# Kernel optimization log

Hardware: AMD Instinct MI355X
Metric: run time of the kernel (lower is better)

Reference implementation:

```python
import jax, jax.numpy as jnp
import numpy as np

N, E = 40000, 640000
EMB, HID, H, TXT = 128, 128, 4, 384
C = HID // H  # per-head channels = 32


def _prelu(x, a):
    return jnp.where(x >= 0, x, a * x)


def _layernorm(x, g, b, eps=1e-5):
    m = jnp.mean(x, axis=-1, keepdims=True)
    v = jnp.mean((x - m) ** 2, axis=-1, keepdims=True)
    return (x - m) / jnp.sqrt(v + eps) * g + b


def _gat_conv(h, src, dst, W, att_src, att_dst, bias):
    # PyG GATConv (concat=True, eval mode): lin has no bias, self-loops already in src/dst.
    xh = (h @ W.T).reshape(N, H, C)                      # [N,H,C]
    a_src = jnp.sum(xh * att_src, axis=-1)               # [N,H]
    a_dst = jnp.sum(xh * att_dst, axis=-1)               # [N,H]
    alpha = jax.nn.leaky_relu(a_src[src] + a_dst[dst], negative_slope=0.2)  # [Et,H]
    amax = jax.ops.segment_max(alpha, dst, num_segments=N)
    ex = jnp.exp(alpha - amax[dst])
    denom = jax.ops.segment_sum(ex, dst, num_segments=N)
    coef = ex / denom[dst]                               # scatter-softmax over dst
    out = jax.ops.segment_sum(xh[src] * coef[:, :, None], dst, num_segments=N)
    return out.reshape(N, H * C) + bias


def setup_inputs() -> dict:
    key = jax.random.key(0)
    ks = jax.random.split(key, 20)
    nrm = lambda k, s, sc=0.05: jax.random.normal(k, s, jnp.float32) * sc
    inp = {
        "x": nrm(ks[0], (N, EMB), 1.0),
        "num_x": nrm(ks[1], (N, 1), 1.0),
        "num_mask": jnp.ones((N,), jnp.float32),
        "txt_x": nrm(ks[2], (N, TXT), 1.0),
        "txt_mask": jnp.ones((N,), jnp.float32),
        "edge_index": jax.random.randint(ks[3], (2, E), 0, N, jnp.int32),
        "num_proj_w": nrm(ks[4], (EMB, 1)), "num_proj_b": jnp.zeros((EMB,), jnp.float32),
        "txt_proj_w": nrm(ks[5], (EMB, TXT)), "txt_proj_b": jnp.zeros((EMB,), jnp.float32),
        "node_proj_w": nrm(ks[6], (HID, EMB)), "node_proj_b": jnp.zeros((HID,), jnp.float32),
        "prelu0_a": jnp.full((HID,), 0.25, jnp.float32),
        "conv1_w": nrm(ks[7], (HID, HID)), "att_src1": nrm(ks[8], (H, C)), "att_dst1": nrm(ks[9], (H, C)), "bias1": jnp.zeros((HID,), jnp.float32),
        "norm1_g": jnp.ones((HID,), jnp.float32), "norm1_b": jnp.zeros((HID,), jnp.float32),
        "prelu1_a": jnp.full((HID,), 0.25, jnp.float32),
        "conv2_w": nrm(ks[10], (HID, HID)), "att_src2": nrm(ks[11], (H, C)), "att_dst2": nrm(ks[12], (H, C)), "bias2": jnp.zeros((HID,), jnp.float32),
        "norm2_g": jnp.ones((HID,), jnp.float32), "norm2_b": jnp.zeros((HID,), jnp.float32),
        "prelu2_a": jnp.full((HID,), 0.25, jnp.float32),
        "out_w": nrm(ks[13], (1, HID)), "out_b": jnp.zeros((1,), jnp.float32),
    }
    return inp


def reference(x, num_x, num_mask, txt_x, txt_mask, edge_index,
              num_proj_w, num_proj_b, txt_proj_w, txt_proj_b,
              node_proj_w, node_proj_b, prelu0_a,
              conv1_w, att_src1, att_dst1, bias1, norm1_g, norm1_b, prelu1_a,
              conv2_w, att_src2, att_dst2, bias2, norm2_g, norm2_b, prelu2_a,
              out_w, out_b):
    # add self loops (PyG GATConv default)
    loop = jnp.arange(N, dtype=edge_index.dtype)
    src = jnp.concatenate([edge_index[0], loop])
    dst = jnp.concatenate([edge_index[1], loop])

    h = (num_x * num_mask[:, None]) @ num_proj_w.T + num_proj_b
    h = h + (txt_x * txt_mask[:, None]) @ txt_proj_w.T + txt_proj_b
    h = h + x @ node_proj_w.T + node_proj_b
    h = _prelu(h, prelu0_a)

    h = _gat_conv(h, src, dst, conv1_w, att_src1, att_dst1, bias1)
    h = _prelu(_layernorm(h, norm1_g, norm1_b), prelu1_a)  # dropout: eval mode -> identity

    h = _gat_conv(h, src, dst, conv2_w, att_src2, att_dst2, bias2)
    h = _prelu(_layernorm(h, norm2_g, norm2_b), prelu2_a)

    return (h @ out_w.T + out_b).squeeze(-1)  # [N]
```

## Files before the change

kernel.cpp:

```cpp
#include <hip/hip_runtime.h>
#include <stdint.h>

typedef unsigned short u16;
typedef unsigned int u32;
typedef __attribute__((ext_vector_type(8))) short bf16x8;
typedef __attribute__((ext_vector_type(4))) float f32x4;

__device__ __forceinline__ float bf2f(u32 u) {
    union { u32 i; float f; } v; v.i = u << 16; return v.f;
}
__device__ __forceinline__ u16 f2bf(float f) {
    u32 x = __float_as_uint(f);
    return (u16)((x + 0x7fffu + ((x >> 16) & 1u)) >> 16);
}
__device__ __forceinline__ float wred_sum(float v) {
#pragma unroll
    for (int o = 32; o > 0; o >>= 1) v += __shfl_xor(v, o, 64);
    return v;
}
__device__ __forceinline__ bf16x8 ldA_f32(const float* p, size_t off) {
    union { uint4 u; bf16x8 b; } t;
    const float* af = p + off;
    float4 a = *(const float4*)af, b2 = *(const float4*)(af + 4);
    t.u.x = (u32)f2bf(a.x)  | ((u32)f2bf(a.y)  << 16);
    t.u.y = (u32)f2bf(a.z)  | ((u32)f2bf(a.w)  << 16);
    t.u.z = (u32)f2bf(b2.x) | ((u32)f2bf(b2.y) << 16);
    t.u.w = (u32)f2bf(b2.z) | ((u32)f2bf(b2.w) << 16);
    return t.b;
}
__device__ __forceinline__ bf16x8 ld16B(const u16* p, size_t off) {
    union { uint4 u; bf16x8 b; } t; t.u = *(const uint4*)(p + off); return t.b;
}
__device__ __forceinline__ bf16x8 ldB(const u16* sw, int ct, int ks, int l16, int quad) {
    union { uint4 u; bf16x8 b; } t;
    t.u = *(const uint4*)&sw[(ct * 16 + l16) * 136 + ks * 32 + quad * 8];
    return t.b;
}
__device__ __forceinline__ void stage256_f32(const float* W, int stride, int koff,
                                             u16* sw, int tid) {
#pragma unroll
    for (int it = 0; it < 8; ++it) {
        int idx = (it * 256 + tid) * 8;
        int c = idx >> 7, kk = idx & 127;
        const float* wf = W + (size_t)c * stride + koff + kk;
        float4 a = *(const float4*)wf, b = *(const float4*)(wf + 4);
        uint4 v;
        v.x = (u32)f2bf(a.x) | ((u32)f2bf(a.y) << 16);
        v.y = (u32)f2bf(a.z) | ((u32)f2bf(a.w) << 16);
        v.z = (u32)f2bf(b.x) | ((u32)f2bf(b.y) << 16);
        v.w = (u32)f2bf(b.z) | ((u32)f2bf(b.w) << 16);
        *(uint4*)&sw[c * 136 + kk] = v;
    }
}

__global__ void k_zero(int* __restrict__ p, int n) {
    int i = blockIdx.x * 256 + threadIdx.x;
    if (i < n) p[i] = 0;
}
__global__ void k_hist(const int* __restrict__ dst, int E, int* __restrict__ deg) {
    int e = blockIdx.x * 256 + threadIdx.x;
    if (e < E) atomicAdd(&deg[dst[e]], 1);
}
__global__ __launch_bounds__(1024) void k_scanA(const int* __restrict__ deg, int n,
                                                int* __restrict__ out, int* __restrict__ bsum) {
    __shared__ int wsum[16];
    int t = threadIdx.x, w = t >> 6, lane = t & 63;
    int i0 = blockIdx.x * 4096 + t * 4;
    int4 v = make_int4(0, 0, 0, 0);
    if (i0 + 3 < n) v = *(const int4*)&deg[i0];
    else {
        if (i0 < n)     v.x = deg[i0];
        if (i0 + 1 < n) v.y = deg[i0 + 1];
        if (i0 + 2 < n) v.z = deg[i0 + 2];
    }
    int tsum = v.x + v.y + v.z + v.w;
    int s = tsum;
#pragma unroll
    for (int o = 1; o < 64; o <<= 1) { int u = __shfl_up(s, o, 64); if (lane >= o) s += u; }
    if (lane == 63) wsum[w] = s;
    __syncthreads();
    if (w == 0 && lane < 16) {
        int ws = wsum[lane];
#pragma unroll
        for (int o = 1; o < 16; o <<= 1) { int u = __shfl_up(ws, o, 64); if (lane >= o) ws += u; }
        wsum[lane] = ws;
    }
    __syncthreads();
    int woff = (w == 0) ? 0 : wsum[w - 1];
    int p = woff + s - tsum;
    if (i0 + 3 < n) {
        int4 o4; o4.x = p; o4.y = p + v.x; o4.z = p + v.x + v.y; o4.w = p + v.x + v.y + v.z;
        *(int4*)&out[i0] = o4;
    } else {
        int pp = p;
        if (i0 < n)     { out[i0] = pp;     pp += v.x; }
        if (i0 + 1 < n) { out[i0 + 1] = pp; pp += v.y; }
        if (i0 + 2 < n) { out[i0 + 2] = pp; }
    }
    if (t == 0) bsum[blockIdx.x] = wsum[15];
}
__global__ void k_scanB(int* __restrict__ bsum, int nb, int* __restrict__ total) {
    int lane = threadIdx.x;
    int v = (lane < nb) ? bsum[lane] : 0;
    int s = v;
#pragma unroll
    for (int o = 1; o < 64; o <<= 1) { int u = __shfl_up(s, o, 64); if (lane >= o) s += u; }
    if (lane < nb) bsum[lane] = s - v;
    if (lane == 63) total[0] = s;
}
__global__ void k_scanC(int* __restrict__ rowptr, int* __restrict__ cursor,
                        const int* __restrict__ boff, int n) {
    int i = blockIdx.x * 256 + threadIdx.x;
    if (i < n) {
        int r = rowptr[i] + boff[i >> 12];
        rowptr[i] = r; cursor[i] = r;
    }
}
__global__ void k_scatter(const int* __restrict__ srcp, const int* __restrict__ dstp, int E,
                          int* __restrict__ cursor, int* __restrict__ col) {
    int e = blockIdx.x * 256 + threadIdx.x;
    if (e < E) {
        int p = atomicAdd(&cursor[dstp[e]], 1);
        col[p] = srcp[e];
    }
}

__global__ __launch_bounds__(256) void k_fused1(
    const float* __restrict__ x, const float* __restrict__ numx, const float* __restrict__ numm,
    const float* __restrict__ txt, const float* __restrict__ txtm,
    const float* __restrict__ numw, const float* __restrict__ numb,
    const float* __restrict__ txtw, const float* __restrict__ txtb,
    const float* __restrict__ nodew, const float* __restrict__ nodeb,
    const float* __restrict__ pa,
    const float* __restrict__ W1, const float* __restrict__ atts, const float* __restrict__ attd,
    u16* __restrict__ xh, float* __restrict__ asrc, float* __restrict__ adst) {
    __shared__ u16 sw[128 * 136];
    __shared__ u16 sh[4][16 * 136];
    int tid = threadIdx.x, w = tid >> 6, lane = tid & 63, quad = lane >> 4, l16 = lane & 15;
    int nb = blockIdx.x * 64 + w * 16;
    f32x4 acc[8];
#pragma unroll
    for (int ct = 0; ct < 8; ++ct) { f32x4 z = {0.f, 0.f, 0.f, 0.f}; acc[ct] = z; }

    for (int chunk = 0; chunk < 3; ++chunk) {
        __syncthreads();
        stage256_f32(txtw, 384, chunk * 128, sw, tid);
        __syncthreads();
#pragma unroll
        for (int ks = 0; ks < 4; ++ks) {
            bf16x8 a0 = ldA_f32(txt, (size_t)(nb + l16) * 384 + chunk * 128 + ks * 32 + quad * 8);
#pragma unroll
            for (int ct = 0; ct < 8; ++ct)
                acc[ct] = __builtin_amdgcn_mfma_f32_16x16x32_bf16(
                    a0, ldB(sw, ct, ks, l16, quad), acc[ct], 0, 0, 0);
        }
    }
#pragma unroll
    for (int r = 0; r < 4; ++r) {
        float tm = txtm[nb + quad * 4 + r];
#pragma unroll
        for (int ct = 0; ct < 8; ++ct) acc[ct][r] *= tm;
    }
    __syncthreads();
    stage256_f32(nodew, 128, 0, sw, tid);
    __syncthreads();
#pragma unroll
    for (int ks = 0; ks < 4; ++ks) {
        bf16x8 a0 = ldA_f32(x, (size_t)(nb + l16) * 128 + ks * 32 + quad * 8);
#pragma unroll
        for (int ct = 0; ct < 8; ++ct)
            acc[ct] = __builtin_amdgcn_mfma_f32_16x16x32_bf16(
                a0, ldB(sw, ct, ks, l16, quad), acc[ct], 0, 0, 0);
    }
    float nm[4];
#pragma unroll
    for (int r = 0; r < 4; ++r) {
        int n = nb + quad * 4 + r;
        nm[r] = numx[n] * numm[n];
    }
#pragma unroll
    for (int ct = 0; ct < 8; ++ct) {
        int c = ct * 16 + l16;
        float cw = numw[c];
        float cb = numb[c] + txtb[c] + nodeb[c];
        float pav = pa[c];
#pragma unroll
        for (int r = 0; r < 4; ++r) {
            float v = acc[ct][r] + nm[r] * cw + cb;
            v = v >= 0.f ? v : pav * v;
            sh[w][(quad * 4 + r) * 136 + c] = f2bf(v);
        }
    }
    __syncthreads();
    stage256_f32(W1, 128, 0, sw, tid);
    __syncthreads();
    f32x4 a2[8];
#pragma unroll
    for (int ct = 0; ct < 8; ++ct) { f32x4 z = {0.f, 0.f, 0.f, 0.f}; a2[ct] = z; }
#pragma unroll
    for (int ks = 0; ks < 4; ++ks) {
        bf16x8 a0 = ld16B(sh[w], l16 * 136 + ks * 32 + quad * 8);
#pragma unroll
        for (int ct = 0; ct < 8; ++ct)
            a2[ct] = __builtin_amdgcn_mfma_f32_16x16x32_bf16(
                a0, ldB(sw, ct, ks, l16, quad), a2[ct], 0, 0, 0);
    }
#pragma unroll
    for (int ct = 0; ct < 8; ++ct) {
        int c = ct * 16 + l16;
#pragma unroll
        for (int r = 0; r < 4; ++r)
            xh[(size_t)(nb + quad * 4 + r) * 128 + c] = f2bf(a2[ct][r]);
    }
    float as_[8], ad_[8];
#pragma unroll
    for (int ct = 0; ct < 8; ++ct) {
        int c = ct * 16 + l16;
        as_[ct] = atts[c];
        ad_[ct] = attd[c];
    }
#pragma unroll
    for (int hh = 0; hh < 4; ++hh) {
        float vs[4], vd[4];
#pragma unroll
        for (int r = 0; r < 4; ++r) {
            vs[r] = a2[2 * hh][r] * as_[2 * hh] + a2[2 * hh + 1][r] * as_[2 * hh + 1];
            vd[r] = a2[2 * hh][r] * ad_[2 * hh] + a2[2 * hh + 1][r] * ad_[2 * hh + 1];
        }
#pragma unroll
        for (int o = 1; o <= 8; o <<= 1) {
#pragma unroll
            for (int r = 0; r < 4; ++r) {
                vs[r] += __shfl_xor(vs[r], o, 64);
                vd[r] += __shfl_xor(vd[r], o, 64);
            }
        }
        if ((l16 >> 2) == hh) {
            int r = l16 & 3;
            float ss = (r == 0) ? vs[0] : (r == 1) ? vs[1] : (r == 2) ? vs[2] : vs[3];
            float dd = (r == 0) ? vd[0] : (r == 1) ? vd[1] : (r == 2) ? vd[2] : vd[3];
            int n = nb + quad * 4 + r;
            asrc[n * 4 + hh] = ss;
            adst[n * 4 + hh] = dd;
        }
    }
}

__global__ __launch_bounds__(256) void k_xh(
    const u16* __restrict__ h, const float* __restrict__ W,
    const float* __restrict__ att_s, const float* __restrict__ att_d,
    u16* __restrict__ xh, float* __restrict__ asrc, float* __restrict__ adst) {
    __shared__ u16 sw[128 * 136];
    int tid = threadIdx.x;
    int w = tid >> 6, lane = tid & 63, quad = lane >> 4, l16 = lane & 15;
    int nb = blockIdx.x * 64 + w * 16;
    f32x4 acc[8];
#pragma unroll
    for (int ct = 0; ct < 8; ++ct) { f32x4 z = {0.f, 0.f, 0.f, 0.f}; acc[ct] = z; }

    stage256_f32(W, 128, 0, sw, tid);
    __syncthreads();
#pragma unroll
    for (int ks = 0; ks < 4; ++ks) {
        bf16x8 a0 = ld16B(h, (size_t)(nb + l16) * 128 + ks * 32 + quad * 8);
#pragma unroll
        for (int ct = 0; ct < 8; ++ct)
            acc[ct] = __builtin_amdgcn_mfma_f32_16x16x32_bf16(
                a0, ldB(sw, ct, ks, l16, quad), acc[ct], 0, 0, 0);
    }
#pragma unroll
    for (int ct = 0; ct < 8; ++ct) {
        int c = ct * 16 + l16;
#pragma unroll
        for (int r = 0; r < 4; ++r) {
            int n = nb + quad * 4 + r;
            xh[(size_t)n * 128 + c] = f2bf(acc[ct][r]);
        }
    }
    float as_[8], ad_[8];
#pragma unroll
    for (int ct = 0; ct < 8; ++ct) {
        int c = ct * 16 + l16;
        as_[ct] = att_s[c];
        ad_[ct] = att_d[c];
    }
#pragma unroll
    for (int hh = 0; hh < 4; ++hh) {
        float vs[4], vd[4];
#pragma unroll
        for (int r = 0; r < 4; ++r) {
            vs[r] = acc[2 * hh][r] * as_[2 * hh] + acc[2 * hh + 1][r] * as_[2 * hh + 1];
            vd[r] = acc[2 * hh][r] * ad_[2 * hh] + acc[2 * hh + 1][r] * ad_[2 * hh + 1];
        }
#pragma unroll
        for (int o = 1; o <= 8; o <<= 1) {
#pragma unroll
            for (int r = 0; r < 4; ++r) {
                vs[r] += __shfl_xor(vs[r], o, 64);
                vd[r] += __shfl_xor(vd[r], o, 64);
            }
        }
        if ((l16 >> 2) == hh) {
            int r = l16 & 3;
            float ss = (r == 0) ? vs[0] : (r == 1) ? vs[1] : (r == 2) ? vs[2] : vs[3];
            float dd = (r == 0) ? vd[0] : (r == 1) ? vd[1] : (r == 2) ? vd[2] : vd[3];
            int n = nb + quad * 4 + r;
            asrc[n * 4 + hh] = ss;
            adst[n * 4 + hh] = dd;
        }
    }
}

__global__ __launch_bounds__(64) void k_agg(
    const u16* __restrict__ xh, const float* __restrict__ asrc, const float* __restrict__ adst,
    const int* __restrict__ rowptr, const int* __restrict__ col,
    const float* __restrict__ bias, const float* __restrict__ g, const float* __restrict__ b,
    const float* __restrict__ pa, u16* __restrict__ hnext,
    const float* __restrict__ outw, const float* __restrict__ outb, float* __restrict__ outy,
    int is_final) {
    __shared__ int   scol[64];
    __shared__ float scoef[64][4];
    int n = blockIdx.x, lane = threadIdx.x;
    int beg = rowptr[n], end = rowptr[n + 1];
    const float4* asrc4 = (const float4*)asrc;

    float4 adv = ((const float4*)adst)[n];
    float ad[4] = { adv.x, adv.y, adv.z, adv.w };
    float4 asv = asrc4[n];
    float els[4];
#pragma unroll
    for (int h = 0; h < 4; h++) {
        float a = ((const float*)&asv)[h] + ad[h];
        a = a >= 0.f ? a : 0.2f * a;
        els[h] = __expf(a);
    }
    int hh = lane >> 4;
    u32 vself = ((const u32*)(xh + (size_t)n * 128))[lane];
    float acc0 = els[hh] * bf2f(vself & 0xffffu);
    float acc1 = els[hh] * bf2f(vself >> 16);
    float a0b = 0.f, a1b = 0.f, a0c = 0.f, a1c = 0.f, a0d = 0.f, a1d = 0.f;
    float l[4] = { 0.f, 0.f, 0.f, 0.f };

    for (int base = beg; base < end; base += 64) {
        int e = base + lane;
        int cnt = min(64, end - base);
        if (e < end) {
            int s = col[e];
            float4 av = asrc4[s];
            scol[lane] = s;
            float cf[4];
#pragma unroll
            for (int h = 0; h < 4; h++) {
                float a = ((const float*)&av)[h] + ad[h];
                a = a >= 0.f ? a : 0.2f * a;
                cf[h] = __expf(a);
                l[h] += cf[h];
            }
            *(float4*)scoef[lane] = make_float4(cf[0], cf[1], cf[2], cf[3]);
        }
        __syncthreads();
        int j = 0;
        for (; j + 3 < cnt; j += 4) {
            int s0 = scol[j], s1 = scol[j + 1], s2 = scol[j + 2], s3 = scol[j + 3];
            float c0 = scoef[j][hh], c1 = scoef[j + 1][hh];
            float c2 = scoef[j + 2][hh], c3 = scoef[j + 3][hh];
            u32 v0 = ((const u32*)(xh + (size_t)s0 * 128))[lane];
            u32 v1 = ((const u32*)(xh + (size_t)s1 * 128))[lane];
            u32 v2 = ((const u32*)(xh + (size_t)s2 * 128))[lane];
            u32 v3 = ((const u32*)(xh + (size_t)s3 * 128))[lane];
            acc0 += c0 * bf2f(v0 & 0xffffu);  acc1 += c0 * bf2f(v0 >> 16);
            a0b  += c1 * bf2f(v1 & 0xffffu);  a1b  += c1 * bf2f(v1 >> 16);
            a0c  += c2 * bf2f(v2 & 0xffffu);  a1c  += c2 * bf2f(v2 >> 16);
            a0d  += c3 * bf2f(v3 & 0xffffu);  a1d  += c3 * bf2f(v3 >> 16);
        }
        for (; j < cnt; ++j) {
            int s0 = scol[j];
            float c0 = scoef[j][hh];
            u32 v0 = ((const u32*)(xh + (size_t)s0 * 128))[lane];
            acc0 += c0 * bf2f(v0 & 0xffffu);
            acc1 += c0 * bf2f(v0 >> 16);
        }
        __syncthreads();
    }
    acc0 += a0b + a0c + a0d;
    acc1 += a1b + a1c + a1d;

    float L[4];
#pragma unroll
    for (int h = 0; h < 4; h++) L[h] = wred_sum(l[h]) + els[h];
    float inv = 1.f / L[hh];
    acc0 *= inv;
    acc1 *= inv;

    int c0i = 2 * lane;
    float2 bi = *(const float2*)(bias + c0i);
    acc0 += bi.x; acc1 += bi.y;

    float mean = wred_sum(acc0 + acc1) * (1.f / 128.f);
    float d0 = acc0 - mean, d1 = acc1 - mean;
    float var = wred_sum(d0 * d0 + d1 * d1) * (1.f / 128.f);
    float rstd = rsqrtf(var + 1e-5f);
    float2 gg = *(const float2*)(g + c0i);
    float2 bb = *(const float2*)(b + c0i);
    float2 pp = *(const float2*)(pa + c0i);
    float y0 = d0 * rstd * gg.x + bb.x;
    float y1 = d1 * rstd * gg.y + bb.y;
    y0 = y0 >= 0.f ? y0 : pp.x * y0;
    y1 = y1 >= 0.f ? y1 : pp.y * y1;

    if (is_final) {
        float2 ow = *(const float2*)(outw + c0i);
        float dot = wred_sum(y0 * ow.x + y1 * ow.y);
        if (lane == 0) outy[n] = dot + outb[0];
    } else {
        ((u32*)(hnext + (size_t)n * 128))[lane] = (u32)f2bf(y0) | ((u32)f2bf(y1) << 16);
    }
}

extern "C" void kernel_launch(void* const* d_in, const int* in_sizes, int n_in,
                              void* d_out, int out_size, void* d_ws, size_t ws_size,
                              hipStream_t stream) {
    const int N = in_sizes[2];
    const int E = in_sizes[5] / 2;

    const float* x      = (const float*)d_in[0];
    const float* numx   = (const float*)d_in[1];
    const float* numm   = (const float*)d_in[2];
    const float* txt    = (const float*)d_in[3];
    const float* txtm   = (const float*)d_in[4];
    const int*   ei     = (const int*)d_in[5];
    const float* numw   = (const float*)d_in[6];
    const float* numb   = (const float*)d_in[7];
    const float* txtw   = (const float*)d_in[8];
    const float* txtb   = (const float*)d_in[9];
    const float* nodew  = (const float*)d_in[10];
    const float* nodeb  = (const float*)d_in[11];
    const float* pa0    = (const float*)d_in[12];
    const float* conv1w = (const float*)d_in[13];
    const float* atts1  = (const float*)d_in[14];
    const float* attd1  = (const float*)d_in[15];
    const float* bias1  = (const float*)d_in[16];
    const float* g1     = (const float*)d_in[17];
    const float* b1     = (const float*)d_in[18];
    const float* pa1    = (const float*)d_in[19];
    const float* conv2w = (const float*)d_in[20];
    const float* atts2  = (const float*)d_in[21];
    const float* attd2  = (const float*)d_in[22];
    const float* bias2  = (const float*)d_in[23];
    const float* g2     = (const float*)d_in[24];
    const float* b2     = (const float*)d_in[25];
    const float* pa2    = (const float*)d_in[26];
    const float* outw   = (const float*)d_in[27];
    const float* outb   = (const float*)d_in[28];

    const int* srcp = ei;
    const int* dstp = ei + E;

    char* p = (char*)d_ws;
    auto alloc = [&](size_t bytes) -> void* {
        void* q = (void*)p;
        p += (bytes + 255) & ~(size_t)255;
        return q;
    };
    u16*   hA     = (u16*)alloc((size_t)N * 128 * 2);
    u16*   hB     = (u16*)alloc((size_t)N * 128 * 2);
    float* asrc   = (float*)alloc((size_t)N * 4 * 4);
    float* adst   = (float*)alloc((size_t)N * 4 * 4);
    int*   deg    = (int*)alloc((size_t)N * 4);
    int*   rowptr = (int*)alloc((size_t)(N + 1) * 4);
    int*   cursor = (int*)alloc((size_t)N * 4);
    int*   col    = (int*)alloc((size_t)E * 4);
    int*   bsum   = (int*)alloc(64 * 4);

    const int nbScan = (N + 4095) / 4096;
    k_zero<<<(N + 255) / 256, 256, 0, stream>>>(deg, N);
    k_hist<<<(E + 255) / 256, 256, 0, stream>>>(dstp, E, deg);
    k_scanA<<<nbScan, 1024, 0, stream>>>(deg, N, rowptr, bsum);
    k_scanB<<<1, 64, 0, stream>>>(bsum, nbScan, rowptr + N);
    k_scanC<<<(N + 255) / 256, 256, 0, stream>>>(rowptr, cursor, bsum, N);
    k_scatter<<<(E + 255) / 256, 256, 0, stream>>>(srcp, dstp, E, cursor, col);

    const int gProj = N / 64;

    k_fused1<<<gProj, 256, 0, stream>>>(x, numx, numm, txt, txtm, numw, numb,
                                        txtw, txtb, nodew, nodeb, pa0,
                                        conv1w, atts1, attd1, hB, asrc, adst);
    k_agg<<<N, 64, 0, stream>>>(hB, asrc, adst, rowptr, col, bias1, g1, b1, pa1,
                                hA, nullptr, nullptr, nullptr, 0);

    k_xh<<<gProj, 256, 0, stream>>>(hA, conv2w, atts2, attd2, hB, asrc, adst);
    k_agg<<<N, 64, 0, stream>>>(hB, asrc, adst, rowptr, col, bias2, g2, b2, pa2,
                                nullptr, outw, outb, (float*)d_out, 1);
}
```

Baseline: 328.9 us.

## Pre-convert weights to bf16 once, prefetch GEMM operands, deepen aggregation gather unroll

A new kernel converts the text, node and both conv weight matrices to bf16 once per call. The projection kernels then stage those bf16 weights from registers, so each block no longer repeats the fp32 load and convert. k_fused1 and k_xh issue all activation and weight loads up front to overlap memory latency with the MFMA work. The aggregation kernel's gather loop is unrolled to 8 independent accumulators to keep more loads in flight. In exchange it adds a kernel launch and raises register pressure, which may lower occupancy.

```diff
diff --git a/kernel.cpp b/kernel.cpp
--- a/kernel.cpp
+++ b/kernel.cpp
@@ -18,15 +18,13 @@
     for (int o = 32; o > 0; o >>= 1) v += __shfl_xor(v, o, 64);
     return v;
 }
-__device__ __forceinline__ bf16x8 ldA_f32(const float* p, size_t off) {
-    union { uint4 u; bf16x8 b; } t;
-    const float* af = p + off;
-    float4 a = *(const float4*)af, b2 = *(const float4*)(af + 4);
-    t.u.x = (u32)f2bf(a.x)  | ((u32)f2bf(a.y)  << 16);
-    t.u.y = (u32)f2bf(a.z)  | ((u32)f2bf(a.w)  << 16);
-    t.u.z = (u32)f2bf(b2.x) | ((u32)f2bf(b2.y) << 16);
-    t.u.w = (u32)f2bf(b2.z) | ((u32)f2bf(b2.w) << 16);
-    return t.b;
+__device__ __forceinline__ bf16x8 cvt8(float4 a, float4 b) {
+    union { uint4 u; bf16x8 v; } t;
+    t.u.x = (u32)f2bf(a.x) | ((u32)f2bf(a.y) << 16);
+    t.u.y = (u32)f2bf(a.z) | ((u32)f2bf(a.w) << 16);
+    t.u.z = (u32)f2bf(b.x) | ((u32)f2bf(b.y) << 16);
+    t.u.w = (u32)f2bf(b.z) | ((u32)f2bf(b.w) << 16);
+    return t.v;
 }
 __device__ __forceinline__ bf16x8 ld16B(const u16* p, size_t off) {
     union { uint4 u; bf16x8 b; } t; t.u = *(const uint4*)(p + off); return t.b;
@@ -36,21 +34,42 @@
     t.u = *(const uint4*)&sw[(ct * 16 + l16) * 136 + ks * 32 + quad * 8];
     return t.b;
 }
-__device__ __forceinline__ void stage256_f32(const float* W, int stride, int koff,
-                                             u16* sw, int tid) {
+__device__ __forceinline__ void ldW8(const u16* __restrict__ W, int ldk, int koff,
+                                     int tid, uint4* r) {
 #pragma unroll
     for (int it = 0; it < 8; ++it) {
         int idx = (it * 256 + tid) * 8;
-        int c = idx >> 7, kk = idx & 127;
-        const float* wf = W + (size_t)c * stride + koff + kk;
-        float4 a = *(const float4*)wf, b = *(const float4*)(wf + 4);
-        uint4 v;
-        v.x = (u32)f2bf(a.x) | ((u32)f2bf(a.y) << 16);
-        v.y = (u32)f2bf(a.z) | ((u32)f2bf(a.w) << 16);
-        v.z = (u32)f2bf(b.x) | ((u32)f2bf(b.y) << 16);
-        v.w = (u32)f2bf(b.z) | ((u32)f2bf(b.w) << 16);
-        *(uint4*)&sw[c * 136 + kk] = v;
-    }
+        int row = idx >> 7, kk = idx & 127;
+        r[it] = *(const uint4*)(W + (size_t)row * ldk + koff + kk);
+    }
+}
+__device__ __forceinline__ void stW8(u16* sw, int tid, const uint4* r) {
+#pragma unroll
+    for (int it = 0; it < 8; ++it) {
+        int idx = (it * 256 + tid) * 8;
+        int row = idx >> 7, kk = idx & 127;
+        *(uint4*)&sw[row * 136 + kk] = r[it];
+    }
+}
+
+__global__ void k_cvtw(const float* __restrict__ s0, const float* __restrict__ s1,
+                       const float* __restrict__ s2, const float* __restrict__ s3,
+                       u16* __restrict__ d, int n0, int n1, int n2, int n3) {
+    int i = (blockIdx.x * 256 + threadIdx.x) * 8;
+    int t = i;
+    const float* s;
+    if (t < n0) s = s0 + t;
+    else if ((t -= n0) < n1) s = s1 + t;
+    else if ((t -= n1) < n2) s = s2 + t;
+    else if ((t -= n2) < n3) s = s3 + t;
+    else return;
+    float4 a = *(const float4*)s, b = *(const float4*)(s + 4);
+    uint4 v;
+    v.x = (u32)f2bf(a.x) | ((u32)f2bf(a.y) << 16);
+    v.y = (u32)f2bf(a.z) | ((u32)f2bf(a.w) << 16);
+    v.z = (u32)f2bf(b.x) | ((u32)f2bf(b.y) << 16);
+    v.w = (u32)f2bf(b.z) | ((u32)f2bf(b.w) << 16);
+    *(uint4*)(d + i) = v;
 }
 
 __global__ void k_zero(int* __restrict__ p, int n) {
@@ -129,31 +148,80 @@
     const float* __restrict__ x, const float* __restrict__ numx, const float* __restrict__ numm,
     const float* __restrict__ txt, const float* __restrict__ txtm,
     const float* __restrict__ numw, const float* __restrict__ numb,
-    const float* __restrict__ txtw, const float* __restrict__ txtb,
-    const float* __restrict__ nodew, const float* __restrict__ nodeb,
+    const float* __restrict__ txtb, const float* __restrict__ nodeb,
     const float* __restrict__ pa,
-    const float* __restrict__ W1, const float* __restrict__ atts, const float* __restrict__ attd,
+    const u16* __restrict__ txtwb, const u16* __restrict__ nodewb, const u16* __restrict__ w1b,
+    const float* __restrict__ atts, const float* __restrict__ attd,
     u16* __restrict__ xh, float* __restrict__ asrc, float* __restrict__ adst) {
     __shared__ u16 sw[128 * 136];
     __shared__ u16 sh[4][16 * 136];
     int tid = threadIdx.x, w = tid >> 6, lane = tid & 63, quad = lane >> 4, l16 = lane & 15;
     int nb = blockIdx.x * 64 + w * 16;
+
+    uint4 wr0[8], wr1[8];
+    ldW8(txtwb, 384, 0, tid, wr0);
+    ldW8(txtwb, 384, 128, tid, wr1);
+
+    float4 At0[8], At1[8], At2[8], Ax[8];
+    const float* trow = txt + (size_t)(nb + l16) * 384;
+    const float* xrow = x + (size_t)(nb + l16) * 128;
+#pragma unroll
+    for (int ks = 0; ks < 4; ++ks) {
+        const float* p0 = trow + ks * 32 + quad * 8;
+        At0[ks * 2] = *(const float4*)p0; At0[ks * 2 + 1] = *(const float4*)(p0 + 4);
+    }
+#pragma unroll
+    for (int ks = 0; ks < 4; ++ks) {
+        const float* p1 = trow + 128 + ks * 32 + quad * 8;
+        At1[ks * 2] = *(const float4*)p1; At1[ks * 2 + 1] = *(const float4*)(p1 + 4);
+    }
+#pragma unroll
+    for (int ks = 0; ks < 4; ++ks) {
+        const float* p2 = trow + 256 + ks * 32 + quad * 8;
+        At2[ks * 2] = *(const float4*)p2; At2[ks * 2 + 1] = *(const float4*)(p2 + 4);
+    }
+#pragma unroll
+    for (int ks = 0; ks < 4; ++ks) {
+        const float* px = xrow + ks * 32 + quad * 8;
+        Ax[ks * 2] = *(const float4*)px; Ax[ks * 2 + 1] = *(const float4*)(px + 4);
+    }
+
     f32x4 acc[8];
 #pragma unroll
     for (int ct = 0; ct < 8; ++ct) { f32x4 z = {0.f, 0.f, 0.f, 0.f}; acc[ct] = z; }
 
-    for (int chunk = 0; chunk < 3; ++chunk) {
-        __syncthreads();
-        stage256_f32(txtw, 384, chunk * 128, sw, tid);
-        __syncthreads();
-#pragma unroll
-        for (int ks = 0; ks < 4; ++ks) {
-            bf16x8 a0 = ldA_f32(txt, (size_t)(nb + l16) * 384 + chunk * 128 + ks * 32 + quad * 8);
-#pragma unroll
-            for (int ct = 0; ct < 8; ++ct)
-                acc[ct] = __builtin_amdgcn_mfma_f32_16x16x32_bf16(
-                    a0, ldB(sw, ct, ks, l16, quad), acc[ct], 0, 0, 0);
-        }
+    stW8(sw, tid, wr0);
+    __syncthreads();
+#pragma unroll
+    for (int ks = 0; ks < 4; ++ks) {
+        bf16x8 a0 = cvt8(At0[ks * 2], At0[ks * 2 + 1]);
+#pragma unroll
+        for (int ct = 0; ct < 8; ++ct)
+            acc[ct] = __builtin_amdgcn_mfma_f32_16x16x32_bf16(
+                a0, ldB(sw, ct, ks, l16, quad), acc[ct], 0, 0, 0);
+    }
+    __syncthreads();
+    stW8(sw, tid, wr1);
+    __syncthreads();
+#pragma unroll
+    for (int ks = 0; ks < 4; ++ks) {
+        bf16x8 a0 = cvt8(At1[ks * 2], At1[ks * 2 + 1]);
+#pragma unroll
+        for (int ct = 0; ct < 8; ++ct)
+            acc[ct] = __builtin_amdgcn_mfma_f32_16x16x32_bf16(
+                a0, ldB(sw, ct, ks, l16, quad), acc[ct], 0, 0, 0);
+    }
+    __syncthreads();
+    ldW8(txtwb, 384, 256, tid, wr0);
+    stW8(sw, tid, wr0);
+    __syncthreads();
+#pragma unroll
+    for (int ks = 0; ks < 4; ++ks) {
+        bf16x8 a0 = cvt8(At2[ks * 2], At2[ks * 2 + 1]);
+#pragma unroll
+        for (int ct = 0; ct < 8; ++ct)
+            acc[ct] = __builtin_amdgcn_mfma_f32_16x16x32_bf16(
+                a0, ldB(sw, ct, ks, l16, quad), acc[ct], 0, 0, 0);
     }
 #pragma unroll
     for (int r = 0; r < 4; ++r) {
@@ -162,11 +230,12 @@
         for (int ct = 0; ct < 8; ++ct) acc[ct][r] *= tm;
     }
     __syncthreads();
-    stage256_f32(nodew, 128, 0, sw, tid);
-    __syncthreads();
-#pragma unroll
-    for (int ks = 0; ks < 4; ++ks) {
-        bf16x8 a0 = ldA_f32(x, (size_t)(nb + l16) * 128 + ks * 32 + quad * 8);
+    ldW8(nodewb, 128, 0, tid, wr0);
+    stW8(sw, tid, wr0);
+    __syncthreads();
+#pragma unroll
+    for (int ks = 0; ks < 4; ++ks) {
+        bf16x8 a0 = cvt8(Ax[ks * 2], Ax[ks * 2 + 1]);
 #pragma unroll
         for (int ct = 0; ct < 8; ++ct)
             acc[ct] = __builtin_amdgcn_mfma_f32_16x16x32_bf16(
@@ -192,7 +261,8 @@
         }
     }
     __syncthreads();
-    stage256_f32(W1, 128, 0, sw, tid);
+    ldW8(w1b, 128, 0, tid, wr0);
+    stW8(sw, tid, wr0);
     __syncthreads();
     f32x4 a2[8];
 #pragma unroll
@@ -247,26 +317,31 @@
 }
 
 __global__ __launch_bounds__(256) void k_xh(
-    const u16* __restrict__ h, const float* __restrict__ W,
+    const u16* __restrict__ h, const u16* __restrict__ Wb,
     const float* __restrict__ att_s, const float* __restrict__ att_d,
     u16* __restrict__ xh, float* __restrict__ asrc, float* __restrict__ adst) {
     __shared__ u16 sw[128 * 136];
     int tid = threadIdx.x;
     int w = tid >> 6, lane = tid & 63, quad = lane >> 4, l16 = lane & 15;
     int nb = blockIdx.x * 64 + w * 16;
+    uint4 wr[8];
+    ldW8(Wb, 128, 0, tid, wr);
+    uint4 Ar[4];
+    const u16* hrow = h + (size_t)(nb + l16) * 128;
+#pragma unroll
+    for (int ks = 0; ks < 4; ++ks) Ar[ks] = *(const uint4*)(hrow + ks * 32 + quad * 8);
     f32x4 acc[8];
 #pragma unroll
     for (int ct = 0; ct < 8; ++ct) { f32x4 z = {0.f, 0.f, 0.f, 0.f}; acc[ct] = z; }
-
-    stage256_f32(W, 128, 0, sw, tid);
-    __syncthreads();
-#pragma unroll
-    for (int ks = 0; ks < 4; ++ks) {
-        bf16x8 a0 = ld16B(h, (size_t)(nb + l16) * 128 + ks * 32 + quad * 8);
+    stW8(sw, tid, wr);
+    __syncthreads();
+#pragma unroll
+    for (int ks = 0; ks < 4; ++ks) {
+        union { uint4 u; bf16x8 b; } t; t.u = Ar[ks];
 #pragma unroll
         for (int ct = 0; ct < 8; ++ct)
             acc[ct] = __builtin_amdgcn_mfma_f32_16x16x32_bf16(
-                a0, ldB(sw, ct, ks, l16, quad), acc[ct], 0, 0, 0);
+                t.b, ldB(sw, ct, ks, l16, quad), acc[ct], 0, 0, 0);
     }
 #pragma unroll
     for (int ct = 0; ct < 8; ++ct) {
@@ -336,9 +411,11 @@
     }
     int hh = lane >> 4;
     u32 vself = ((const u32*)(xh + (size_t)n * 128))[lane];
-    float acc0 = els[hh] * bf2f(vself & 0xffffu);
-    float acc1 = els[hh] * bf2f(vself >> 16);
-    float a0b = 0.f, a1b = 0.f, a0c = 0.f, a1c = 0.f, a0d = 0.f, a1d = 0.f;
+    float ac0[8], ac1[8];
+#pragma unroll
+    for (int q = 0; q < 8; ++q) { ac0[q] = 0.f; ac1[q] = 0.f; }
+    ac0[0] = els[hh] * bf2f(vself & 0xffffu);
+    ac1[0] = els[hh] * bf2f(vself >> 16);
     float l[4] = { 0.f, 0.f, 0.f, 0.f };
 
     for (int base = beg; base < end; base += 64) {
@@ -360,30 +437,42 @@
         }
         __syncthreads();
         int j = 0;
+        for (; j + 7 < cnt; j += 8) {
+            int ss[8]; float cc[8]; u32 vv[8];
+#pragma unroll
+            for (int q = 0; q < 8; ++q) { ss[q] = scol[j + q]; cc[q] = scoef[j + q][hh]; }
+#pragma unroll
+            for (int q = 0; q < 8; ++q) vv[q] = ((const u32*)(xh + (size_t)ss[q] * 128))[lane];
+#pragma unroll
+            for (int q = 0; q < 8; ++q) {
+                ac0[q] += cc[q] * bf2f(vv[q] & 0xffffu);
+                ac1[q] += cc[q] * bf2f(vv[q] >> 16);
+            }
+        }
         for (; j + 3 < cnt; j += 4) {
-            int s0 = scol[j], s1 = scol[j + 1], s2 = scol[j + 2], s3 = scol[j + 3];
-            float c0 = scoef[j][hh], c1 = scoef[j + 1][hh];
-            float c2 = scoef[j + 2][hh], c3 = scoef[j + 3][hh];
-            u32 v0 = ((const u32*)(xh + (size_t)s0 * 128))[lane];
-            u32 v1 = ((const u32*)(xh + (size_t)s1 * 128))[lane];
-            u32 v2 = ((const u32*)(xh + (size_t)s2 * 128))[lane];
-            u32 v3 = ((const u32*)(xh + (size_t)s3 * 128))[lane];
-            acc0 += c0 * bf2f(v0 & 0xffffu);  acc1 += c0 * bf2f(v0 >> 16);
-            a0b  += c1 * bf2f(v1 & 0xffffu);  a1b  += c1 * bf2f(v1 >> 16);
-            a0c  += c2 * bf2f(v2 & 0xffffu);  a1c  += c2 * bf2f(v2 >> 16);
-            a0d  += c3 * bf2f(v3 & 0xffffu);  a1d  += c3 * bf2f(v3 >> 16);
+            int ss[4]; float cc[4]; u32 vv[4];
+#pragma unroll
+            for (int q = 0; q < 4; ++q) { ss[q] = scol[j + q]; cc[q] = scoef[j + q][hh]; }
+#pragma unroll
+            for (int q = 0; q < 4; ++q) vv[q] = ((const u32*)(xh + (size_t)ss[q] * 128))[lane];
+#pragma unroll
+            for (int q = 0; q < 4; ++q) {
+                ac0[q] += cc[q] * bf2f(vv[q] & 0xffffu);
+                ac1[q] += cc[q] * bf2f(vv[q] >> 16);
+            }
         }
         for (; j < cnt; ++j) {
             int s0 = scol[j];
             float c0 = scoef[j][hh];
             u32 v0 = ((const u32*)(xh + (size_t)s0 * 128))[lane];
-            acc0 += c0 * bf2f(v0 & 0xffffu);
-            acc1 += c0 * bf2f(v0 >> 16);
+            ac0[0] += c0 * bf2f(v0 & 0xffffu);
+            ac1[0] += c0 * bf2f(v0 >> 16);
         }
         __syncthreads();
     }
-    acc0 += a0b + a0c + a0d;
-    acc1 += a1b + a1c + a1d;
+    float acc0 = 0.f, acc1 = 0.f;
+#pragma unroll
+    for (int q = 0; q < 8; ++q) { acc0 += ac0[q]; acc1 += ac1[q]; }
 
     float L[4];
 #pragma unroll
@@ -456,6 +545,12 @@
     const int* srcp = ei;
     const int* dstp = ei + E;
 
+    const int szTxtw = in_sizes[8];
+    const int szNode = in_sizes[10];
+    const int szW1   = in_sizes[13];
+    const int szW2   = in_sizes[20];
+    const int szWAll = szTxtw + szNode + szW1 + szW2;
+
     char* p = (char*)d_ws;
     auto alloc = [&](size_t bytes) -> void* {
         void* q = (void*)p;
@@ -471,6 +566,15 @@
     int*   cursor = (int*)alloc((size_t)N * 4);
     int*   col    = (int*)alloc((size_t)E * 4);
     int*   bsum   = (int*)alloc(64 * 4);
+    u16*   wbf    = (u16*)alloc((size_t)szWAll * 2);
+
+    u16* txtwb  = wbf;
+    u16* nodewb = wbf + szTxtw;
+    u16* w1b    = nodewb + szNode;
+    u16* w2b    = w1b + szW1;
+
+    k_cvtw<<<(szWAll / 8 + 255) / 256, 256, 0, stream>>>(
+        txtw, nodew, conv1w, conv2w, wbf, szTxtw, szNode, szW1, szW2);
 
     const int nbScan = (N + 4095) / 4096;
     k_zero<<<(N + 255) / 256, 256, 0, stream>>>(deg, N);
@@ -483,12 +587,12 @@
     const int gProj = N / 64;
 
     k_fused1<<<gProj, 256, 0, stream>>>(x, numx, numm, txt, txtm, numw, numb,
-                                        txtw, txtb, nodew, nodeb, pa0,
-                                        conv1w, atts1, attd1, hB, asrc, adst);
+                                        txtb, nodeb, pa0,
+                                        txtwb, nodewb, w1b, atts1, attd1, hB, asrc, adst);
     k_agg<<<N, 64, 0, stream>>>(hB, asrc, adst, rowptr, col, bias1, g1, b1, pa1,
                                 hA, nullptr, nullptr, nullptr, 0);
 
-    k_xh<<<gProj, 256, 0, stream>>>(hA, conv2w, atts2, attd2, hB, asrc, adst);
+    k_xh<<<gProj, 256, 0, stream>>>(hA, w2b, atts2, attd2, hB, asrc, adst);
     k_agg<<<N, 64, 0, stream>>>(hB, asrc, adst, rowptr, col, bias2, g2, b2, pa2,
                                 nullptr, outw, outb, (float*)d_out, 1);
 }
```

Result: no change. 325.1 us (-1.1%).
